# Optimization experiments

Measured on AMD Instinct MI355X. Metric: run time of the kernel, lower is better.

Reference implementation:

```python
import jax, jax.numpy as jnp
import numpy as np

H = 128  # hidden_size

def _lstm_layer(x, w_ih, w_hh, b_ih, b_hh):
    # x: [B, T, D]; w_ih: [4H, D]; w_hh: [4H, H]; biases: [4H]
    B, T, _ = x.shape
    # Precompute input contributions for all timesteps (the big GEMM).
    xg = jnp.einsum('btd,gd->btg', x, w_ih) + b_ih + b_hh  # [B, T, 4H]
    xg = jnp.transpose(xg, (1, 0, 2))  # [T, B, 4H]
    w_hh_t = w_hh.T  # [H, 4H]

    def step(carry, xt):
        h, c = carry
        g = xt + h @ w_hh_t  # [B, 4H]
        i, f, gg, o = jnp.split(g, 4, axis=-1)  # PyTorch gate order i,f,g,o
        i = jax.nn.sigmoid(i)
        f = jax.nn.sigmoid(f)
        gg = jnp.tanh(gg)
        o = jax.nn.sigmoid(o)
        c = f * c + i * gg
        h = o * jnp.tanh(c)
        return (h, c), h

    h0 = jnp.zeros((B, H), dtype=x.dtype)
    c0 = jnp.zeros((B, H), dtype=x.dtype)
    _, hs = jax.lax.scan(step, (h0, c0), xg)  # hs: [T, B, H]
    return jnp.transpose(hs, (1, 0, 2))  # [B, T, H]

def setup_inputs() -> dict:
    key = jax.random.key(0)
    ks = jax.random.split(key, 11)
    s = 1.0 / np.sqrt(H)  # PyTorch LSTM init scale
    return {
        'x': jax.random.normal(ks[0], (128, 512, 1024), dtype=jnp.float32),
        'w_ih0': jax.random.normal(ks[1], (4 * H, 1024), dtype=jnp.float32) * s,
        'w_hh0': jax.random.normal(ks[2], (4 * H, H), dtype=jnp.float32) * s,
        'b_ih0': jax.random.normal(ks[3], (4 * H,), dtype=jnp.float32) * s,
        'b_hh0': jax.random.normal(ks[4], (4 * H,), dtype=jnp.float32) * s,
        'w_ih1': jax.random.normal(ks[5], (4 * H, H), dtype=jnp.float32) * s,
        'w_hh1': jax.random.normal(ks[6], (4 * H, H), dtype=jnp.float32) * s,
        'b_ih1': jax.random.normal(ks[7], (4 * H,), dtype=jnp.float32) * s,
        'b_hh1': jax.random.normal(ks[8], (4 * H,), dtype=jnp.float32) * s,
        'fc_w': jax.random.normal(ks[9], (8, H), dtype=jnp.float32) * s,
        'fc_b': jax.random.normal(ks[10], (8,), dtype=jnp.float32) * s,
    }

def reference(x, w_ih0, w_hh0, b_ih0, b_hh0, w_ih1, w_hh1, b_ih1, b_hh1, fc_w, fc_b):
    h1 = _lstm_layer(x, w_ih0, w_hh0, b_ih0, b_hh0)   # [B, T, H]
    h2 = _lstm_layer(h1, w_ih1, w_hh1, b_ih1, b_hh1)  # [B, T, H]
    logits = h2[:, -1, :] @ fc_w.T + fc_b             # [B, num_classes]
    return logits
```

## Files before the change

kernel.cpp:

```cpp
#include <hip/hip_runtime.h>
#include <hip/hip_bf16.h>

#define BATCH 128
#define TSTEPS 512
#define HID 128
#define GATES 512
#define M_TOTAL (BATCH * TSTEPS)

typedef _Float16 h2_t  __attribute__((ext_vector_type(2)));
typedef _Float16 half4 __attribute__((ext_vector_type(4)));
typedef _Float16 half8 __attribute__((ext_vector_type(8)));
typedef float    f32x4 __attribute__((ext_vector_type(4)));

__device__ __forceinline__ float sigmoidf_fast(float x) {
    return 1.0f / (1.0f + __expf(-x));
}
__device__ __forceinline__ float tanhf_fast(float x) {
    return 1.0f - 2.0f / (__expf(2.0f * x) + 1.0f);
}
__device__ __forceinline__ float fdot2h(h2_t a, h2_t b, float c) {
#if __has_builtin(__builtin_amdgcn_fdot2)
    return __builtin_amdgcn_fdot2(a, b, c, false);
#else
    return c + (float)a[0] * (float)b[0] + (float)a[1] * (float)b[1];
#endif
}

__global__ __launch_bounds__(256) void convert_w(
    const float* __restrict__ src, _Float16* __restrict__ hi, _Float16* __restrict__ lo)
{
    const int i = blockIdx.x * 256 + threadIdx.x;
    float4 v = ((const float4*)src)[i];
    half4 h, l;
    h[0] = (_Float16)v.x; l[0] = (_Float16)(v.x - (float)h[0]);
    h[1] = (_Float16)v.y; l[1] = (_Float16)(v.y - (float)h[1]);
    h[2] = (_Float16)v.z; l[2] = (_Float16)(v.z - (float)h[2]);
    h[3] = (_Float16)v.w; l[3] = (_Float16)(v.w - (float)h[3]);
    *(half4*)&hi[4 * i] = h;
    *(half4*)&lo[4 * i] = l;
}

__global__ __launch_bounds__(256, 2) void gemm_mfma(
    const float* __restrict__ A,
    const _Float16* __restrict__ Wh,
    const _Float16* __restrict__ Wl,
    const float* __restrict__ b0,
    const float* __restrict__ b1,
    float* __restrict__ xg)
{
    constexpr int K = 1024;
    __shared__ __align__(16) _Float16 sXh[128 * 32];
    __shared__ __align__(16) _Float16 sXl[128 * 32];
    __shared__ __align__(16) _Float16 sWh[128 * 32];
    __shared__ __align__(16) _Float16 sWl[128 * 32];

    const int tid = threadIdx.x;
    const int lane = tid & 63, wv = tid >> 6;
    const int wm = wv & 1, wn = wv >> 1;
    const int n0 = blockIdx.x * 128;
    const int m0 = blockIdx.y * 128;

    const int ar = tid & 127, aks = (tid >> 7) * 16;
    const float* pA = A + (size_t)(m0 + ar) * K + aks;
    const _Float16* pWh0 = Wh + (size_t)(n0 + (tid & 127)) * K + (tid >> 7) * 8;
    const _Float16* pWl0 = Wl + (size_t)(n0 + (tid & 127)) * K + (tid >> 7) * 8;

    f32x4 acc[4][4];
    #pragma unroll
    for (int nt = 0; nt < 4; ++nt) {
        const int cn = n0 + wn * 64 + nt * 16 + (lane & 15);
        const float bv = b0[cn] + b1[cn];
        #pragma unroll
        for (int mt = 0; mt < 4; ++mt) acc[mt][nt] = (f32x4){bv, bv, bv, bv};
    }

    float xv[16];
    half8 w0h, w1h, w0l, w1l;
    #pragma unroll
    for (int j = 0; j < 4; ++j) *(float4*)&xv[4 * j] = *(const float4*)(pA + 4 * j);
    w0h = *(const half8*)(pWh0);      w1h = *(const half8*)(pWh0 + 16);
    w0l = *(const half8*)(pWl0);      w1l = *(const half8*)(pWl0 + 16);

    const int kb0 = (tid >> 7) * 2;
    for (int ks = 0; ks < 32; ++ks) {
        half8 hh0, hh1, hl0, hl1;
        #pragma unroll
        for (int j = 0; j < 8; ++j) {
            _Float16 h = (_Float16)xv[j];
            hh0[j] = h; hl0[j] = (_Float16)(xv[j] - (float)h);
        }
        #pragma unroll
        for (int j = 0; j < 8; ++j) {
            _Float16 h = (_Float16)xv[8 + j];
            hh1[j] = h; hl1[j] = (_Float16)(xv[8 + j] - (float)h);
        }
        if (ks) __syncthreads();
        *(half8*)&sXh[(size_t)((kb0    ) * 128 + ar) * 8] = hh0;
        *(half8*)&sXh[(size_t)((kb0 + 1) * 128 + ar) * 8] = hh1;
        *(half8*)&sXl[(size_t)((kb0    ) * 128 + ar) * 8] = hl0;
        *(half8*)&sXl[(size_t)((kb0 + 1) * 128 + ar) * 8] = hl1;
        *(half8*)&sWh[(size_t)tid * 8]         = w0h;
        *(half8*)&sWh[(size_t)(tid + 256) * 8] = w1h;
        *(half8*)&sWl[(size_t)tid * 8]         = w0l;
        *(half8*)&sWl[(size_t)(tid + 256) * 8] = w1l;
        __syncthreads();

        if (ks < 31) {
            const int kn = (ks + 1) * 32;
            #pragma unroll
            for (int j = 0; j < 4; ++j)
                *(float4*)&xv[4 * j] = *(const float4*)(pA + kn + 4 * j);
            w0h = *(const half8*)(pWh0 + kn);      w1h = *(const half8*)(pWh0 + kn + 16);
            w0l = *(const half8*)(pWl0 + kn);      w1l = *(const half8*)(pWl0 + kn + 16);
        }

        const int fr = lane & 15, kb = lane >> 4;
        half8 ah[4], al[4], bh[4], bl[4];
        #pragma unroll
        for (int mt = 0; mt < 4; ++mt) {
            const int idx = (kb * 128 + wm * 64 + mt * 16 + fr) * 8;
            ah[mt] = *(const half8*)&sXh[idx];
            al[mt] = *(const half8*)&sXl[idx];
        }
        #pragma unroll
        for (int nt = 0; nt < 4; ++nt) {
            const int idx = (kb * 128 + wn * 64 + nt * 16 + fr) * 8;
            bh[nt] = *(const half8*)&sWh[idx];
            bl[nt] = *(const half8*)&sWl[idx];
        }
        #pragma unroll
        for (int mt = 0; mt < 4; ++mt)
            #pragma unroll
            for (int nt = 0; nt < 4; ++nt) {
                acc[mt][nt] = __builtin_amdgcn_mfma_f32_16x16x32_f16(ah[mt], bh[nt], acc[mt][nt], 0, 0, 0);
                acc[mt][nt] = __builtin_amdgcn_mfma_f32_16x16x32_f16(ah[mt], bl[nt], acc[mt][nt], 0, 0, 0);
                acc[mt][nt] = __builtin_amdgcn_mfma_f32_16x16x32_f16(al[mt], bh[nt], acc[mt][nt], 0, 0, 0);
            }
    }

    #pragma unroll
    for (int mt = 0; mt < 4; ++mt) {
        const int rm = m0 + wm * 64 + mt * 16 + (lane >> 4) * 4;
        #pragma unroll
        for (int nt = 0; nt < 4; ++nt) {
            const int cn = n0 + wn * 64 + nt * 16 + (lane & 15);
            #pragma unroll
            for (int r = 0; r < 4; ++r)
                xg[(size_t)(rm + r) * GATES + cn] = acc[mt][nt][r];
        }
    }
}

__global__ __launch_bounds__(512, 1) void fused_rec2(
    const float* __restrict__ xg,
    const float* __restrict__ w_hh0,
    const float* __restrict__ w_ih1,
    const float* __restrict__ w_hh1,
    const float* __restrict__ b_ih1,
    const float* __restrict__ b_hh1,
    const float* __restrict__ fc_w,
    const float* __restrict__ fc_b,
    unsigned int* __restrict__ h1g,
    int* __restrict__ flags,
    float* __restrict__ logits)
{
    const int blk = blockIdx.x;
    const bool L1 = blk >= BATCH;
    const int b = blk & (BATCH - 1);
    const int tid = threadIdx.x;
    const int ks = tid >> 7;
    const int gq = tid & 127;

    __shared__ __align__(16) _Float16 h16[HID];
    __shared__ __align__(16) float part[128 * 20];
    __shared__ __align__(16) unsigned int hin[8][64];
    __shared__ __align__(16) float hfin[HID];

    h2_t wh[4][16], wi[4][16];
    {
        const float* wsrc = (L1 ? w_hh1 : w_hh0);
        #pragma unroll
        for (int q = 0; q < 4; ++q) {
            const float4* w4 = (const float4*)(wsrc + (size_t)(gq + 128 * q) * HID + 32 * ks);
            #pragma unroll
            for (int i = 0; i < 8; ++i) {
                float4 v = w4[i];
                wh[q][2 * i]     = (h2_t){(_Float16)v.x, (_Float16)v.y};
                wh[q][2 * i + 1] = (h2_t){(_Float16)v.z, (_Float16)v.w};
            }
        }
    }
    float bias = 0.f;
    if (L1) {
        #pragma unroll
        for (int q = 0; q < 4; ++q) {
            const float4* w4 = (const float4*)(w_ih1 + (size_t)(gq + 128 * q) * HID + 32 * ks);
            #pragma unroll
            for (int i = 0; i < 8; ++i) {
                float4 v = w4[i];
                wi[q][2 * i]     = (h2_t){(_Float16)v.x, (_Float16)v.y};
                wi[q][2 * i + 1] = (h2_t){(_Float16)v.z, (_Float16)v.w};
            }
        }
        bias = b_ih1[tid] + b_hh1[tid];
    }

    if (tid < HID) h16[tid] = (_Float16)0.f;
    float c = 0.f;

    unsigned int* h1row = h1g + (size_t)b * TSTEPS * 64;
    int* flagb = flags + b * 64;

    if (L1 && tid < 64) {
        while (__hip_atomic_load(&flagb[tid], __ATOMIC_ACQUIRE, __HIP_MEMORY_SCOPE_AGENT) < 8) {}
        #pragma unroll
        for (int d = 0; d < 8; ++d)
            hin[d][tid] = __hip_atomic_load(&h1row[(size_t)d * 64 + tid],
                                            __ATOMIC_RELAXED, __HIP_MEMORY_SCOPE_AGENT);
    }

    const float* xgb = xg + (size_t)b * TSTEPS * GATES + tid;
    float xcur[4], xnxt[4];
    if (!L1) {
        #pragma unroll
        for (int u = 0; u < 4; ++u) xcur[u] = xgb[(size_t)u * GATES];
    }
    __syncthreads();

    for (int t4 = 0; t4 < 128; ++t4) {
        if (!L1) {
            const int tn = (t4 + 1 < 128) ? (t4 + 1) * 4 : t4 * 4;
            #pragma unroll
            for (int u = 0; u < 4; ++u) xnxt[u] = xgb[(size_t)(tn + u) * GATES];
        }
        #pragma unroll
        for (int u = 0; u < 4; ++u) {
            const int t = t4 * 4 + u;
            float p0 = 0.f, p1 = 0.f, p2 = 0.f, p3 = 0.f;
            {
                const half8* hv8 = ((const half8*)h16) + 4 * ks;
                #pragma unroll
                for (int jj = 0; jj < 4; ++jj) {
                    half8 hh = hv8[jj];
                    #pragma unroll
                    for (int e = 0; e < 4; ++e) {
                        h2_t hp = (h2_t){hh[2 * e], hh[2 * e + 1]};
                        p0 = fdot2h(wh[0][4 * jj + e], hp, p0);
                        p1 = fdot2h(wh[1][4 * jj + e], hp, p1);
                        p2 = fdot2h(wh[2][4 * jj + e], hp, p2);
                        p3 = fdot2h(wh[3][4 * jj + e], hp, p3);
                    }
                }
            }
            if (L1) {
                float q0 = 0.f, q1 = 0.f, q2 = 0.f, q3 = 0.f;
                const half8* xv8 = ((const half8*)&hin[t & 7][0]) + 4 * ks;
                #pragma unroll
                for (int jj = 0; jj < 4; ++jj) {
                    half8 hh = xv8[jj];
                    #pragma unroll
                    for (int e = 0; e < 4; ++e) {
                        h2_t hp = (h2_t){hh[2 * e], hh[2 * e + 1]};
                        q0 = fdot2h(wi[0][4 * jj + e], hp, q0);
                        q1 = fdot2h(wi[1][4 * jj + e], hp, q1);
                        q2 = fdot2h(wi[2][4 * jj + e], hp, q2);
                        q3 = fdot2h(wi[3][4 * jj + e], hp, q3);
                    }
                }
                p0 += q0; p1 += q1; p2 += q2; p3 += q3;
            }
            {
                const float extra = L1 ? bias : xcur[u];
                if      (ks == 0) p0 += extra;
                else if (ks == 1) p1 += extra;
                else if (ks == 2) p2 += extra;
                else              p3 += extra;
            }
            *(f32x4*)&part[gq * 20 + ks * 4] = (f32x4){p0, p1, p2, p3};
            __syncthreads();
            if (tid < HID) {
                const f32x4* pr = (const f32x4*)&part[tid * 20];
                f32x4 v0 = pr[0], v1 = pr[1], v2 = pr[2], v3 = pr[3];
                const float si = (v0[0] + v1[0]) + (v2[0] + v3[0]);
                const float sf = (v0[1] + v1[1]) + (v2[1] + v3[1]);
                const float sg = (v0[2] + v1[2]) + (v2[2] + v3[2]);
                const float so = (v0[3] + v1[3]) + (v2[3] + v3[3]);
                const float ig = sigmoidf_fast(si);
                const float fg = sigmoidf_fast(sf);
                const float gg = tanhf_fast(sg);
                const float og = sigmoidf_fast(so);
                c = __fmaf_rn(fg, c, ig * gg);
                const float h = og * tanhf_fast(c);
                h16[tid] = (_Float16)h;
                if (L1 && t == TSTEPS - 1) hfin[tid] = h;
            }
            __syncthreads();
            if (!L1 && tid < 64) {
                __hip_atomic_store(&h1row[(size_t)t * 64 + tid], ((const unsigned int*)h16)[tid],
                                   __ATOMIC_RELAXED, __HIP_MEMORY_SCOPE_AGENT);
                if (u == 3)
                    __hip_atomic_store(&flagb[tid], t + 1,
                                       __ATOMIC_RELEASE, __HIP_MEMORY_SCOPE_AGENT);
            }
            if (L1 && tid < 64 && u == 3) {
                const int tgt = t + 5;
                if (tgt + 3 < TSTEPS) {
                    while (__hip_atomic_load(&flagb[tid], __ATOMIC_ACQUIRE,
                                             __HIP_MEMORY_SCOPE_AGENT) < tgt + 4) {}
                    #pragma unroll
                    for (int d = 0; d < 4; ++d)
                        hin[(tgt + d) & 7][tid] =
                            __hip_atomic_load(&h1row[(size_t)(tgt + d) * 64 + tid],
                                              __ATOMIC_RELAXED, __HIP_MEMORY_SCOPE_AGENT);
                }
            }
        }
        if (!L1) {
            xcur[0] = xnxt[0]; xcur[1] = xnxt[1]; xcur[2] = xnxt[2]; xcur[3] = xnxt[3];
        }
    }

    if (L1) {
        __syncthreads();
        if (tid < 8) {
            float s2 = fc_b[tid];
            const float* wr = fc_w + tid * HID;
            #pragma unroll 4
            for (int k2 = 0; k2 < HID; ++k2) s2 = __fmaf_rn(wr[k2], hfin[k2], s2);
            logits[b * 8 + tid] = s2;
        }
    }
}

extern "C" void kernel_launch(void* const* d_in, const int* in_sizes, int n_in,
                              void* d_out, int out_size, void* d_ws, size_t ws_size,
                              hipStream_t stream) {
    const float* x     = (const float*)d_in[0];
    const float* w_ih0 = (const float*)d_in[1];
    const float* w_hh0 = (const float*)d_in[2];
    const float* b_ih0 = (const float*)d_in[3];
    const float* b_hh0 = (const float*)d_in[4];
    const float* w_ih1 = (const float*)d_in[5];
    const float* w_hh1 = (const float*)d_in[6];
    const float* b_ih1 = (const float*)d_in[7];
    const float* b_hh1 = (const float*)d_in[8];
    const float* fc_w  = (const float*)d_in[9];
    const float* fc_b  = (const float*)d_in[10];
    float* out = (float*)d_out;

    char* ws = (char*)d_ws;
    float*        xgb   = (float*)ws;
    _Float16*     Whp   = (_Float16*)(ws + (size_t)M_TOTAL * GATES * 4);
    _Float16*     Wlp   = (_Float16*)(ws + (size_t)M_TOTAL * GATES * 4 + 1048576);
    unsigned int* h1g   = (unsigned int*)(ws + (size_t)M_TOTAL * GATES * 4 + 2097152);
    int*          flags = (int*)(ws + (size_t)M_TOTAL * GATES * 4 + 2097152
                                    + (size_t)BATCH * TSTEPS * 64 * 4);

    convert_w<<<dim3(512), dim3(256), 0, stream>>>(w_ih0, Whp, Wlp);
    gemm_mfma<<<dim3(4, 512), dim3(256), 0, stream>>>(x, Whp, Wlp, b_ih0, b_hh0, xgb);
    fused_rec2<<<dim3(2 * BATCH), dim3(512), 0, stream>>>(
        xgb, w_hh0, w_ih1, w_hh1, b_ih1, b_hh1, fc_w, fc_b, h1g, flags, out);
}
```

Before: 1.498 ms.

## Split recurrent dot products across 1024 threads with eight-way K reduction

The fused two-layer recurrence kernel now launches 1024 threads per block, and the hidden dimension is split into eight slices of 16 instead of four slices of 32. This halves each thread's serial fdot2 chain and its weight register footprint. The price is an eight-way partial-sum reduction in shared memory and barriers that must synchronise twice as many waves every timestep. Empty inline asm pins the fp16 weights in VGPRs so the compiler does not rematerialise or spill them.

```diff
diff --git a/kernel.cpp b/kernel.cpp
--- a/kernel.cpp
+++ b/kernel.cpp
@@ -24,6 +24,11 @@
 #else
     return c + (float)a[0] * (float)b[0] + (float)a[1] * (float)b[1];
 #endif
+}
+__device__ __forceinline__ void pin_h2(h2_t& v) {
+    unsigned u = __builtin_bit_cast(unsigned, v);
+    asm volatile("" : "+v"(u));
+    v = __builtin_bit_cast(h2_t, u);
 }
 
 __global__ __launch_bounds__(256) void convert_w(
@@ -151,7 +156,7 @@
     }
 }
 
-__global__ __launch_bounds__(512, 1) void fused_rec2(
+__global__ __launch_bounds__(1024, 1) void fused_rec2(
     const float* __restrict__ xg,
     const float* __restrict__ w_hh0,
     const float* __restrict__ w_ih1,
@@ -170,39 +175,44 @@
     const int tid = threadIdx.x;
     const int ks = tid >> 7;
     const int gq = tid & 127;
+    const bool owns = (ks < 4);
 
     __shared__ __align__(16) _Float16 h16[HID];
-    __shared__ __align__(16) float part[128 * 20];
+    __shared__ __align__(16) float part[128 * 36];
     __shared__ __align__(16) unsigned int hin[8][64];
     __shared__ __align__(16) float hfin[HID];
 
-    h2_t wh[4][16], wi[4][16];
+    h2_t wh[4][8], wi[4][8];
     {
         const float* wsrc = (L1 ? w_hh1 : w_hh0);
         #pragma unroll
         for (int q = 0; q < 4; ++q) {
-            const float4* w4 = (const float4*)(wsrc + (size_t)(gq + 128 * q) * HID + 32 * ks);
-            #pragma unroll
-            for (int i = 0; i < 8; ++i) {
+            const float4* w4 = (const float4*)(wsrc + (size_t)(gq + 128 * q) * HID + 16 * ks);
+            #pragma unroll
+            for (int i = 0; i < 4; ++i) {
                 float4 v = w4[i];
                 wh[q][2 * i]     = (h2_t){(_Float16)v.x, (_Float16)v.y};
                 wh[q][2 * i + 1] = (h2_t){(_Float16)v.z, (_Float16)v.w};
             }
+            #pragma unroll
+            for (int i = 0; i < 8; ++i) pin_h2(wh[q][i]);
         }
     }
     float bias = 0.f;
     if (L1) {
         #pragma unroll
         for (int q = 0; q < 4; ++q) {
-            const float4* w4 = (const float4*)(w_ih1 + (size_t)(gq + 128 * q) * HID + 32 * ks);
-            #pragma unroll
-            for (int i = 0; i < 8; ++i) {
+            const float4* w4 = (const float4*)(w_ih1 + (size_t)(gq + 128 * q) * HID + 16 * ks);
+            #pragma unroll
+            for (int i = 0; i < 4; ++i) {
                 float4 v = w4[i];
                 wi[q][2 * i]     = (h2_t){(_Float16)v.x, (_Float16)v.y};
                 wi[q][2 * i + 1] = (h2_t){(_Float16)v.z, (_Float16)v.w};
             }
-        }
-        bias = b_ih1[tid] + b_hh1[tid];
+            #pragma unroll
+            for (int i = 0; i < 8; ++i) pin_h2(wi[q][i]);
+        }
+        if (owns) bias = b_ih1[tid] + b_hh1[tid];
     }
 
     if (tid < HID) h16[tid] = (_Float16)0.f;
@@ -221,14 +231,14 @@
 
     const float* xgb = xg + (size_t)b * TSTEPS * GATES + tid;
     float xcur[4], xnxt[4];
-    if (!L1) {
+    if (!L1 && owns) {
         #pragma unroll
         for (int u = 0; u < 4; ++u) xcur[u] = xgb[(size_t)u * GATES];
     }
     __syncthreads();
 
     for (int t4 = 0; t4 < 128; ++t4) {
-        if (!L1) {
+        if (!L1 && owns) {
             const int tn = (t4 + 1 < 128) ? (t4 + 1) * 4 : t4 * 4;
             #pragma unroll
             for (int u = 0; u < 4; ++u) xnxt[u] = xgb[(size_t)(tn + u) * GATES];
@@ -238,9 +248,9 @@
             const int t = t4 * 4 + u;
             float p0 = 0.f, p1 = 0.f, p2 = 0.f, p3 = 0.f;
             {
-                const half8* hv8 = ((const half8*)h16) + 4 * ks;
+                const half8* hv8 = ((const half8*)h16) + 2 * ks;
                 #pragma unroll
-                for (int jj = 0; jj < 4; ++jj) {
+                for (int jj = 0; jj < 2; ++jj) {
                     half8 hh = hv8[jj];
                     #pragma unroll
                     for (int e = 0; e < 4; ++e) {
@@ -254,9 +264,9 @@
             }
             if (L1) {
                 float q0 = 0.f, q1 = 0.f, q2 = 0.f, q3 = 0.f;
-                const half8* xv8 = ((const half8*)&hin[t & 7][0]) + 4 * ks;
+                const half8* xv8 = ((const half8*)&hin[t & 7][0]) + 2 * ks;
                 #pragma unroll
-                for (int jj = 0; jj < 4; ++jj) {
+                for (int jj = 0; jj < 2; ++jj) {
                     half8 hh = xv8[jj];
                     #pragma unroll
                     for (int e = 0; e < 4; ++e) {
@@ -269,26 +279,24 @@
                 }
                 p0 += q0; p1 += q1; p2 += q2; p3 += q3;
             }
-            {
+            if (owns) {
                 const float extra = L1 ? bias : xcur[u];
                 if      (ks == 0) p0 += extra;
                 else if (ks == 1) p1 += extra;
                 else if (ks == 2) p2 += extra;
                 else              p3 += extra;
             }
-            *(f32x4*)&part[gq * 20 + ks * 4] = (f32x4){p0, p1, p2, p3};
+            *(f32x4*)&part[gq * 36 + ks * 4] = (f32x4){p0, p1, p2, p3};
             __syncthreads();
             if (tid < HID) {
-                const f32x4* pr = (const f32x4*)&part[tid * 20];
-                f32x4 v0 = pr[0], v1 = pr[1], v2 = pr[2], v3 = pr[3];
-                const float si = (v0[0] + v1[0]) + (v2[0] + v3[0]);
-                const float sf = (v0[1] + v1[1]) + (v2[1] + v3[1]);
-                const float sg = (v0[2] + v1[2]) + (v2[2] + v3[2]);
-                const float so = (v0[3] + v1[3]) + (v2[3] + v3[3]);
-                const float ig = sigmoidf_fast(si);
-                const float fg = sigmoidf_fast(sf);
-                const float gg = tanhf_fast(sg);
-                const float og = sigmoidf_fast(so);
+                const f32x4* pr = (const f32x4*)&part[tid * 36];
+                f32x4 s = pr[0];
+                #pragma unroll
+                for (int d = 1; d < 8; ++d) { f32x4 v = pr[d]; s[0]+=v[0]; s[1]+=v[1]; s[2]+=v[2]; s[3]+=v[3]; }
+                const float ig = sigmoidf_fast(s[0]);
+                const float fg = sigmoidf_fast(s[1]);
+                const float gg = tanhf_fast(s[2]);
+                const float og = sigmoidf_fast(s[3]);
                 c = __fmaf_rn(fg, c, ig * gg);
                 const float h = og * tanhf_fast(c);
                 h16[tid] = (_Float16)h;
@@ -315,7 +323,7 @@
                 }
             }
         }
-        if (!L1) {
+        if (!L1 && owns) {
             xcur[0] = xnxt[0]; xcur[1] = xnxt[1]; xcur[2] = xnxt[2]; xcur[3] = xnxt[3];
         }
     }
@@ -358,6 +366,6 @@
 
     convert_w<<<dim3(512), dim3(256), 0, stream>>>(w_ih0, Whp, Wlp);
     gemm_mfma<<<dim3(4, 512), dim3(256), 0, stream>>>(x, Whp, Wlp, b_ih0, b_hh0, xgb);
-    fused_rec2<<<dim3(2 * BATCH), dim3(512), 0, stream>>>(
+    fused_rec2<<<dim3(2 * BATCH), dim3(1024), 0, stream>>>(
         xgb, w_hh0, w_ih1, w_hh1, b_ih1, b_hh1, fc_w, fc_b, h1g, flags, out);
 }
```

New measurement: 1.444 ms. -3.6%, faster.
